# Performance work log

Measured on AMD Instinct MI355X. Metric: run time of the kernel, lower is better.

The kernel has to match this reference:

```python
import jax, jax.numpy as jnp
import numpy as np

V = 50257   # n_unique_words
C = 50257   # n_classes
E = 256     # embed_dim
H = 512     # h_dim
S_IN = 512
S_OUT = 511
START = 1


def setup_inputs() -> dict:
    key = jax.random.key(0)
    ks = jax.random.split(key, 12)
    s = 1.0 / np.sqrt(H)
    u = lambda k, shp: jax.random.uniform(k, shp, jnp.float32, -s, s)
    return {
        "h0": jnp.zeros((1, H), jnp.float32),
        "input_ids": jax.random.randint(ks[0], (1, S_IN), 0, V),
        "output_ids": jax.random.randint(ks[1], (1, S_OUT), 0, V),
        "emb": jax.random.normal(ks[2], (V, E), jnp.float32) * 0.02,
        "enc_wih": u(ks[3], (H, E)),
        "enc_whh": u(ks[4], (H, H)),
        "enc_bih": u(ks[5], (H,)),
        "enc_bhh": u(ks[5], (H,)),
        "dec_wih": u(ks[6], (H, E)),
        "dec_whh": u(ks[7], (H, H)),
        "dec_bih": u(ks[8], (H,)),
        "dec_bhh": u(ks[8], (H,)),
        "fc_w": u(ks[9], (C, H)),
        "fc_b": u(ks[10], (C,)),
    }


def _rnn_cell(x, h, wih, whh, bih, bhh):
    # Elman RNNCell: h' = tanh(x W_ih^T + b_ih + h W_hh^T + b_hh)
    return jnp.tanh(x @ wih.T + bih + h @ whh.T + bhh)


def reference(h0, input_ids, output_ids, emb, enc_wih, enc_whh, enc_bih, enc_bhh,
              dec_wih, dec_whh, dec_bih, dec_bhh, fc_w, fc_b):
    # ---- encode ----
    enc_xs = jnp.swapaxes(emb[input_ids], 0, 1)  # [S_in, 1, E]
    def enc_step(h, x):
        h = _rnn_cell(x, h, enc_wih, enc_whh, enc_bih, enc_bhh)
        return h, None
    hn, _ = jax.lax.scan(enc_step, h0, enc_xs)
    # ---- decode_train ----
    start_emb = emb[jnp.array([START])]          # [1, E]
    h1 = _rnn_cell(start_emb, hn, dec_wih, dec_whh, dec_bih, dec_bhh)
    dec_xs = jnp.swapaxes(emb[output_ids], 0, 1)  # [S_out, 1, E]
    def dec_step(h, x):
        h = _rnn_cell(x, h, dec_wih, dec_whh, dec_bih, dec_bhh)
        return h, h
    _, hs = jax.lax.scan(dec_step, h1, dec_xs)    # [S_out, 1, H]
    pred = jnp.concatenate([h1[None], hs], axis=0)[:, 0, :]  # [S_out+1, H]
    return pred @ fc_w.T + fc_b                   # [S_out+1, C]
```

## Files before the change

kernel.cpp:

```cpp
#include <hip/hip_runtime.h>
#include <hip/hip_fp16.h>

#define EDIM 256
#define HDIM 512
#define CDIM 50257

using half2_t = __attribute__((ext_vector_type(2))) _Float16;
using half8_t = __attribute__((ext_vector_type(8))) _Float16;
using float4_t = __attribute__((ext_vector_type(4))) float;

__device__ __forceinline__ float dot2(uint32_t w, uint32_t h, float acc) {
    return __builtin_amdgcn_fdot2(__builtin_bit_cast(half2_t, w),
                                  __builtin_bit_cast(half2_t, h), acc, false);
}

__global__ void __launch_bounds__(256) pack_whh(const float* __restrict__ whh,
                                                _Float16* __restrict__ wpack) {
    int idx = blockIdx.x * blockDim.x + threadIdx.x;
    int g = idx >> 9, t = idx & 511;
    int row = ((t >> 3) << 3) + (g >> 3);
    int k0 = ((t & 7) << 6) + ((g & 7) << 3);
    const float* src = whh + row * HDIM + k0;
    uint32_t d[4];
#pragma unroll
    for (int q = 0; q < 4; ++q) {
        half2_t p;
        p[0] = (_Float16)src[2 * q];
        p[1] = (_Float16)src[2 * q + 1];
        d[q] = __builtin_bit_cast(uint32_t, p);
    }
    uint4 v = make_uint4(d[0], d[1], d[2], d[3]);
    ((uint4*)wpack)[g * 512 + t] = v;
}

__global__ void __launch_bounds__(256) zker(const int* __restrict__ in_ids,
                                            const int* __restrict__ out_ids,
                                            const float* __restrict__ emb,
                                            const float* __restrict__ enc_wih,
                                            const float* __restrict__ enc_bih,
                                            const float* __restrict__ enc_bhh,
                                            const float* __restrict__ dec_wih,
                                            const float* __restrict__ dec_bih,
                                            const float* __restrict__ dec_bhh,
                                            float* __restrict__ z) {
    int t = blockIdx.x;
    const float *wih, *bih, *bhh;
    int id;
    if (t < 512) {
        wih = enc_wih; bih = enc_bih; bhh = enc_bhh; id = in_ids[t];
    } else {
        wih = dec_wih; bih = dec_bih; bhh = dec_bhh;
        id = (t == 512) ? 1 : out_ids[t - 513];
    }
    __shared__ float x[EDIM];
    x[threadIdx.x] = emb[(long)id * EDIM + threadIdx.x];
    __syncthreads();
#pragma unroll
    for (int rr = 0; rr < 2; ++rr) {
        int r = threadIdx.x + rr * 256;
        const float4* w4 = (const float4*)(wih + r * EDIM);
        float acc = 0.f;
#pragma unroll 8
        for (int k4 = 0; k4 < 64; ++k4) {
            float4 wv = w4[k4];
            acc += wv.x * x[k4 * 4 + 0] + wv.y * x[k4 * 4 + 1] +
                   wv.z * x[k4 * 4 + 2] + wv.w * x[k4 * 4 + 3];
        }
        z[t * HDIM + r] = acc + bih[r] + bhh[r];
    }
}

__global__ void __launch_bounds__(512, 2) scan_ker(
    const _Float16* __restrict__ wpack,
    const float* __restrict__ z,
    const _Float16* __restrict__ h_init,
    _Float16* __restrict__ hs_out,
    _Float16* __restrict__ hfin_out,
    int nsteps) {
    __shared__ uint4 wlds[16 * 512];
    __shared__ uint4 hbuf[2][64];

    const int tid = threadIdx.x;
    const int c = tid & 7;
    const int c_of = tid >> 6;
    const int i_of = (tid >> 3) & 7;
    const int hphys = (c_of << 3) | (i_of ^ c_of);

    const uint4* wp4 = (const uint4*)wpack;
    uint32_t wreg[192];
#pragma unroll
    for (int g = 0; g < 48; ++g) {
        uint4 v = wp4[g * 512 + tid];
        wreg[g * 4 + 0] = v.x; wreg[g * 4 + 1] = v.y;
        wreg[g * 4 + 2] = v.z; wreg[g * 4 + 3] = v.w;
    }
#pragma unroll
    for (int g = 48; g < 64; ++g) wlds[(g - 48) * 512 + tid] = wp4[g * 512 + tid];

    {
        _Float16 hv = (_Float16)0.f;
        if (h_init) hv = h_init[tid];
        ((_Float16*)hbuf[0])[hphys * 8 + (tid & 7)] = hv;
    }
    __syncthreads();

    int cur = 0;
    for (int t = 0; t < nsteps; ++t) {
        float zv = z[t * HDIM + tid];
        const uint4* hb = hbuf[cur];
        float acc[8] = {0.f, 0.f, 0.f, 0.f, 0.f, 0.f, 0.f, 0.f};
#pragma unroll
        for (int i = 0; i < 8; ++i) {
            uint4 hg = hb[(c << 3) | (i ^ c)];
#pragma unroll
            for (int jr = 0; jr < 6; ++jr) {
                acc[jr] = dot2(wreg[(jr * 8 + i) * 4 + 0], hg.x, acc[jr]);
                acc[jr] = dot2(wreg[(jr * 8 + i) * 4 + 1], hg.y, acc[jr]);
                acc[jr] = dot2(wreg[(jr * 8 + i) * 4 + 2], hg.z, acc[jr]);
                acc[jr] = dot2(wreg[(jr * 8 + i) * 4 + 3], hg.w, acc[jr]);
            }
            uint4 w6 = wlds[i * 512 + tid];
            uint4 w7 = wlds[(8 + i) * 512 + tid];
            acc[6] = dot2(w6.x, hg.x, acc[6]);
            acc[6] = dot2(w6.y, hg.y, acc[6]);
            acc[6] = dot2(w6.z, hg.z, acc[6]);
            acc[6] = dot2(w6.w, hg.w, acc[6]);
            acc[7] = dot2(w7.x, hg.x, acc[7]);
            acc[7] = dot2(w7.y, hg.y, acc[7]);
            acc[7] = dot2(w7.z, hg.z, acc[7]);
            acc[7] = dot2(w7.w, hg.w, acc[7]);
        }
        float s, keep, b0, b1, b2, b3, d0, d1, v;
#define FOLD(aL, aH, bit, mask, dst)            \
        s = (c & bit) ? (aL) : (aH);            \
        s = __shfl_xor(s, mask, 64);            \
        keep = (c & bit) ? (aH) : (aL);         \
        dst = keep + s;
        FOLD(acc[0], acc[1], 1, 1, b0)
        FOLD(acc[2], acc[3], 1, 1, b1)
        FOLD(acc[4], acc[5], 1, 1, b2)
        FOLD(acc[6], acc[7], 1, 1, b3)
        FOLD(b0, b1, 2, 2, d0)
        FOLD(b2, b3, 2, 2, d1)
        FOLD(d0, d1, 4, 4, v)
#undef FOLD
        float hnew = tanhf(v + zv);
        _Float16 h16v = (_Float16)hnew;
        ((_Float16*)hbuf[cur ^ 1])[hphys * 8 + (tid & 7)] = h16v;
        if (hs_out) hs_out[t * HDIM + tid] = h16v;
        if (hfin_out && t == nsteps - 1) hfin_out[tid] = h16v;
        __syncthreads();
        cur ^= 1;
    }
}

__global__ void __launch_bounds__(256) fc_ker(const _Float16* __restrict__ A,
                                              const float* __restrict__ Bw,
                                              const float* __restrict__ bias,
                                              float* __restrict__ out) {
    int n0 = blockIdx.x * 128, m0 = blockIdx.y * 128;
    int w = threadIdx.x >> 6, l = threadIdx.x & 63;
    int wm = (w >> 1) * 64, wn = (w & 1) * 64;
    int lr = l & 15, lk = (l >> 4) * 8;

    float4_t acc[4][4];
#pragma unroll
    for (int fm = 0; fm < 4; ++fm)
#pragma unroll
        for (int fn = 0; fn < 4; ++fn) acc[fm][fn] = (float4_t){0.f, 0.f, 0.f, 0.f};

    for (int ks = 0; ks < 512; ks += 32) {
        half8_t a[4], b[4];
#pragma unroll
        for (int f = 0; f < 4; ++f) {
            int m = m0 + wm + f * 16 + lr;
            a[f] = *(const half8_t*)(A + (long)m * 512 + ks + lk);
            int n = n0 + wn + f * 16 + lr;
            half8_t bb;
            if (n < CDIM) {
                const float4* bp4 = (const float4*)(Bw + (long)n * 512 + ks + lk);
                float4 x0 = bp4[0], x1 = bp4[1];
                bb[0] = (_Float16)x0.x; bb[1] = (_Float16)x0.y;
                bb[2] = (_Float16)x0.z; bb[3] = (_Float16)x0.w;
                bb[4] = (_Float16)x1.x; bb[5] = (_Float16)x1.y;
                bb[6] = (_Float16)x1.z; bb[7] = (_Float16)x1.w;
            } else {
#pragma unroll
                for (int e = 0; e < 8; ++e) bb[e] = (_Float16)0.f;
            }
            b[f] = bb;
        }
#pragma unroll
        for (int fm = 0; fm < 4; ++fm)
#pragma unroll
            for (int fn = 0; fn < 4; ++fn)
                acc[fm][fn] = __builtin_amdgcn_mfma_f32_16x16x32_f16(
                    a[fm], b[fn], acc[fm][fn], 0, 0, 0);
    }
#pragma unroll
    for (int fn = 0; fn < 4; ++fn) {
        int n = n0 + wn + fn * 16 + lr;
        if (n >= CDIM) continue;
        float bv = bias[n];
#pragma unroll
        for (int fm = 0; fm < 4; ++fm) {
#pragma unroll
            for (int q = 0; q < 4; ++q) {
                int m = m0 + wm + fm * 16 + (l >> 4) * 4 + q;
                out[(long)m * CDIM + n] = acc[fm][fn][q] + bv;
            }
        }
    }
}

extern "C" void kernel_launch(void* const* d_in, const int* in_sizes, int n_in,
                              void* d_out, int out_size, void* d_ws, size_t ws_size,
                              hipStream_t stream) {
    const int* input_ids  = (const int*)d_in[1];
    const int* output_ids = (const int*)d_in[2];
    const float* emb      = (const float*)d_in[3];
    const float* enc_wih  = (const float*)d_in[4];
    const float* enc_whh  = (const float*)d_in[5];
    const float* enc_bih  = (const float*)d_in[6];
    const float* enc_bhh  = (const float*)d_in[7];
    const float* dec_wih  = (const float*)d_in[8];
    const float* dec_whh  = (const float*)d_in[9];
    const float* dec_bih  = (const float*)d_in[10];
    const float* dec_bhh  = (const float*)d_in[11];
    const float* fc_w     = (const float*)d_in[12];
    const float* fc_b     = (const float*)d_in[13];
    float* out = (float*)d_out;

    char* ws = (char*)d_ws;
    float* z        = (float*)ws;
    _Float16* wpe   = (_Float16*)(ws + (2u << 20));
    _Float16* wpd   = (_Float16*)(ws + (2u << 20) + (512u << 10));
    _Float16* h16   = (_Float16*)(ws + (3u << 20));
    _Float16* hn16  = (_Float16*)(ws + (3u << 20) + (512u << 10));

    pack_whh<<<128, 256, 0, stream>>>(enc_whh, wpe);
    pack_whh<<<128, 256, 0, stream>>>(dec_whh, wpd);
    zker<<<1024, 256, 0, stream>>>(input_ids, output_ids, emb,
                                   enc_wih, enc_bih, enc_bhh,
                                   dec_wih, dec_bih, dec_bhh, z);
    scan_ker<<<1, 512, 0, stream>>>(wpe, z, nullptr, nullptr, hn16, 512);
    scan_ker<<<1, 512, 0, stream>>>(wpd, z + 512 * HDIM, hn16, h16, nullptr, 512);
    fc_ker<<<dim3((CDIM + 127) / 128, 4), 256, 0, stream>>>(h16, fc_w, fc_b, out);
}
```

Baseline: 1.678 ms.

## Pre-convert FC weights to fp16 and stream one scan weight slice from global

```diff
diff --git a/kernel.cpp b/kernel.cpp
--- a/kernel.cpp
+++ b/kernel.cpp
@@ -77,7 +77,7 @@
     _Float16* __restrict__ hs_out,
     _Float16* __restrict__ hfin_out,
     int nsteps) {
-    __shared__ uint4 wlds[16 * 512];
+    __shared__ uint4 wlds[8 * 512];
     __shared__ uint4 hbuf[2][64];
 
     const int tid = threadIdx.x;
@@ -95,7 +95,8 @@
         wreg[g * 4 + 2] = v.z; wreg[g * 4 + 3] = v.w;
     }
 #pragma unroll
-    for (int g = 48; g < 64; ++g) wlds[(g - 48) * 512 + tid] = wp4[g * 512 + tid];
+    for (int g = 48; g < 56; ++g) wlds[(g - 48) * 512 + tid] = wp4[g * 512 + tid];
+    const uint4* w7p = wp4 + 56 * 512 + tid;
 
     {
         _Float16 hv = (_Float16)0.f;
@@ -111,6 +112,7 @@
         float acc[8] = {0.f, 0.f, 0.f, 0.f, 0.f, 0.f, 0.f, 0.f};
 #pragma unroll
         for (int i = 0; i < 8; ++i) {
+            uint4 w7 = w7p[i * 512];
             uint4 hg = hb[(c << 3) | (i ^ c)];
 #pragma unroll
             for (int jr = 0; jr < 6; ++jr) {
@@ -120,7 +122,6 @@
                 acc[jr] = dot2(wreg[(jr * 8 + i) * 4 + 3], hg.w, acc[jr]);
             }
             uint4 w6 = wlds[i * 512 + tid];
-            uint4 w7 = wlds[(8 + i) * 512 + tid];
             acc[6] = dot2(w6.x, hg.x, acc[6]);
             acc[6] = dot2(w6.y, hg.y, acc[6]);
             acc[6] = dot2(w6.z, hg.z, acc[6]);
@@ -154,6 +155,73 @@
     }
 }
 
+__global__ void __launch_bounds__(256) cvt_w16(const float* __restrict__ src,
+                                               _Float16* __restrict__ dst, long n) {
+    long i = ((long)blockIdx.x * 256 + threadIdx.x) * 8;
+    if (i + 8 <= n) {
+        const float4* s4 = (const float4*)(src + i);
+        float4 a = s4[0], b = s4[1];
+        half8_t o;
+        o[0] = (_Float16)a.x; o[1] = (_Float16)a.y;
+        o[2] = (_Float16)a.z; o[3] = (_Float16)a.w;
+        o[4] = (_Float16)b.x; o[5] = (_Float16)b.y;
+        o[6] = (_Float16)b.z; o[7] = (_Float16)b.w;
+        *(half8_t*)(dst + i) = o;
+    }
+}
+
+__global__ void __launch_bounds__(256) fc_ker16(const _Float16* __restrict__ A,
+                                                const _Float16* __restrict__ Bw,
+                                                const float* __restrict__ bias,
+                                                float* __restrict__ out) {
+    int n0 = blockIdx.x * 128, m0 = blockIdx.y * 128;
+    int w = threadIdx.x >> 6, l = threadIdx.x & 63;
+    int wm = (w >> 1) * 64, wn = (w & 1) * 64;
+    int lr = l & 15, lk = (l >> 4) * 8;
+
+    float4_t acc[4][4];
+#pragma unroll
+    for (int fm = 0; fm < 4; ++fm)
+#pragma unroll
+        for (int fn = 0; fn < 4; ++fn) acc[fm][fn] = (float4_t){0.f, 0.f, 0.f, 0.f};
+
+    for (int ks = 0; ks < 512; ks += 32) {
+        half8_t a[4], b[4];
+#pragma unroll
+        for (int f = 0; f < 4; ++f) {
+            int m = m0 + wm + f * 16 + lr;
+            a[f] = *(const half8_t*)(A + (long)m * 512 + ks + lk);
+            int n = n0 + wn + f * 16 + lr;
+            if (n < CDIM) {
+                b[f] = *(const half8_t*)(Bw + (long)n * 512 + ks + lk);
+            } else {
+#pragma unroll
+                for (int e = 0; e < 8; ++e) b[f][e] = (_Float16)0.f;
+            }
+        }
+#pragma unroll
+        for (int fm = 0; fm < 4; ++fm)
+#pragma unroll
+            for (int fn = 0; fn < 4; ++fn)
+                acc[fm][fn] = __builtin_amdgcn_mfma_f32_16x16x32_f16(
+                    a[fm], b[fn], acc[fm][fn], 0, 0, 0);
+    }
+#pragma unroll
+    for (int fn = 0; fn < 4; ++fn) {
+        int n = n0 + wn + fn * 16 + lr;
+        if (n >= CDIM) continue;
+        float bv = bias[n];
+#pragma unroll
+        for (int fm = 0; fm < 4; ++fm) {
+#pragma unroll
+            for (int q = 0; q < 4; ++q) {
+                int m = m0 + wm + fm * 16 + (l >> 4) * 4 + q;
+                out[(long)m * CDIM + n] = acc[fm][fn][q] + bv;
+            }
+        }
+    }
+}
+
 __global__ void __launch_bounds__(256) fc_ker(const _Float16* __restrict__ A,
                                               const float* __restrict__ Bw,
                                               const float* __restrict__ bias,
@@ -237,13 +305,24 @@
     _Float16* wpd   = (_Float16*)(ws + (2u << 20) + (512u << 10));
     _Float16* h16   = (_Float16*)(ws + (3u << 20));
     _Float16* hn16  = (_Float16*)(ws + (3u << 20) + (512u << 10));
+    _Float16* fcw16 = (_Float16*)(ws + (4u << 20));
+
+    const long fcw_n = (long)CDIM * HDIM;
+    bool use_f16_fc = ws_size >= (size_t)(4u << 20) + (size_t)fcw_n * 2;
 
     pack_whh<<<128, 256, 0, stream>>>(enc_whh, wpe);
     pack_whh<<<128, 256, 0, stream>>>(dec_whh, wpd);
+    if (use_f16_fc) {
+        int nb = (int)((fcw_n / 8 + 255) / 256);
+        cvt_w16<<<nb, 256, 0, stream>>>(fc_w, fcw16, fcw_n);
+    }
     zker<<<1024, 256, 0, stream>>>(input_ids, output_ids, emb,
                                    enc_wih, enc_bih, enc_bhh,
                                    dec_wih, dec_bih, dec_bhh, z);
     scan_ker<<<1, 512, 0, stream>>>(wpe, z, nullptr, nullptr, hn16, 512);
     scan_ker<<<1, 512, 0, stream>>>(wpd, z + 512 * HDIM, hn16, h16, nullptr, 512);
-    fc_ker<<<dim3((CDIM + 127) / 128, 4), 256, 0, stream>>>(h16, fc_w, fc_b, out);
-}
+    if (use_f16_fc)
+        fc_ker16<<<dim3((CDIM + 127) / 128, 4), 256, 0, stream>>>(h16, fcw16, fc_b, out);
+    else
+        fc_ker<<<dim3((CDIM + 127) / 128, 4), 256, 0, stream>>>(h16, fc_w, fc_b, out);
+}
```

Result: slower. 2.021 ms (+20.4%).
